# Performance work log

Hardware: AMD Instinct MI355X
Metric: run time of the kernel (lower is better)

Reference implementation:

```python
import jax, jax.numpy as jnp
import numpy as np

N_ANCHORS = 200000
TOPK = 4096          # pre-NMS top-k (standard detector practice, fixed output shape)
CONF_T = 0.5
IOU_T = 0.6


def setup_inputs() -> dict:
    key = jax.random.key(0)
    k1, k2, k3 = jax.random.split(key, 3)
    # build valid xyxy boxes: random centers in a 1024x1024 image, sizes 4..128
    cxcy = jax.random.uniform(k1, (1, N_ANCHORS, 2), minval=0.0, maxval=1024.0)
    wh = jax.random.uniform(k2, (1, N_ANCHORS, 2), minval=4.0, maxval=128.0)
    boxes = jnp.concatenate([cxcy - wh / 2, cxcy + wh / 2], axis=-1)  # [1,N,4]
    confs = jax.random.uniform(k3, (1, N_ANCHORS))                    # [1,N]
    return {"boxes": boxes, "confs": confs}


def _pairwise_iou(b):
    # b: [K,4] xyxy -> iou: [K,K]
    area = jnp.clip(b[:, 2] - b[:, 0], 0.0) * jnp.clip(b[:, 3] - b[:, 1], 0.0)
    lt = jnp.maximum(b[:, None, :2], b[None, :, :2])
    rb = jnp.minimum(b[:, None, 2:], b[None, :, 2:])
    wh = jnp.clip(rb - lt, 0.0)
    inter = wh[..., 0] * wh[..., 1]
    return inter / (area[:, None] + area[None, :] - inter + 1e-9)


def reference(boxes, confs):
    b = boxes[0]          # [N,4] single batch (module is single-batch single-class)
    c = confs[0]          # [N]
    # confidence threshold mask; invalid scores pushed below any valid score
    scores = jnp.where(c >= CONF_T, c, -1.0)
    top_scores, idx = jax.lax.top_k(scores, TOPK)   # sorted descending
    top_boxes = b[idx]                              # [K,4]
    iou = _pairwise_iou(top_boxes)                  # [K,K]
    valid_k = top_scores >= CONF_T

    # greedy sequential NMS over score-sorted candidates
    def body(i, state):
        keep, sup = state
        is_keep = jnp.logical_not(sup[i])
        keep = keep.at[i].set(is_keep)
        sup = sup | (is_keep & (iou[i] > IOU_T))
        return (keep, sup)

    keep0 = jnp.zeros((TOPK,), dtype=bool)
    keep, _ = jax.lax.fori_loop(0, TOPK, body, (keep0, jnp.logical_not(valid_k)))

    # [K,5] = x1,y1,x2,y2,conf ; suppressed rows zeroed (fixed output shape)
    out = jnp.concatenate([top_boxes, top_scores[:, None]], axis=-1)
    return jnp.where(keep[:, None], out, 0.0)
```

## Files before the change

kernel.cpp:

```cpp
#include <hip/hip_runtime.h>

#define NTOP   4096
#define SORTN  8192
#define CONF_T 0.5f
#define IOU_T  0.6f

#define HIST_OFF   0
#define CUT_OFF    8192
#define CNT_OFF    8196
#define COMP_OFF   16384
#define MEMSET_BYTES 81920
#define KEYS_OFF   131072
#define TB_OFF     2097152
#define TC_OFF     2162688
#define VALID_OFF  2179072
#define KEEP_OFF   2179584
#define MASK_OFF   4194304

typedef unsigned long long u64;
typedef unsigned int u32;

__device__ __forceinline__ void gload_lds16(const void* g, void* l) {
    __builtin_amdgcn_global_load_lds(
        (const __attribute__((address_space(1))) unsigned int*)g,
        (__attribute__((address_space(3))) unsigned int*)l, 16, 0, 0);
}

__global__ void k_keys(const float* __restrict__ confs, u64* __restrict__ keys,
                       u32* __restrict__ hist, int n) {
    int i = blockIdx.x * 256 + threadIdx.x;
    if (i >= n) return;
    float s = confs[i];
    if (s >= CONF_T) {
        u32 u = __float_as_uint(s);
        keys[i] = ((u64)u << 32) | (u32)(~i);
        int bin = (int)(u >> 12) - 0x3F000;
        bin = bin < 0 ? 0 : (bin > 2047 ? 2047 : bin);
        atomicAdd(&hist[bin], 1u);
    } else {
        keys[i] = 0ull;
    }
}

__global__ __launch_bounds__(256) void k_findcut(const u32* __restrict__ hist,
                                                 int* __restrict__ cut) {
    __shared__ u32 ch[256];
    int t = threadIdx.x;
    u32 h[8]; u32 s = 0;
#pragma unroll
    for (int k = 0; k < 8; ++k) { h[k] = hist[t * 8 + k]; s += h[k]; }
    ch[t] = s;
    __syncthreads();
    for (int off = 1; off < 256; off <<= 1) {
        u32 v = ch[t];
        u32 add = (t + off < 256) ? ch[t + off] : 0u;
        __syncthreads();
        ch[t] = v + add;
        __syncthreads();
    }
    u32 incl = ch[t];
    u32 above = incl - s;
    if (above < NTOP && incl >= NTOP) {
        u32 cum = above; int c = 0;
        for (int k = 7; k >= 0; --k) {
            cum += h[k];
            if (cum >= NTOP) { c = t * 8 + k; break; }
        }
        *cut = c;
    }
    if (t == 0 && ch[0] < NTOP) *cut = 0;
}

__global__ void k_compact(const u64* __restrict__ keys, const int* __restrict__ cut,
                          u64* __restrict__ comp, u32* __restrict__ counter, int n) {
    int i = blockIdx.x * 256 + threadIdx.x;
    if (i >= n) return;
    u64 key = keys[i];
    if (!key) return;
    int bin = (int)(u32)(key >> 44) - 0x3F000;
    bin = bin < 0 ? 0 : (bin > 2047 ? 2047 : bin);
    if (bin >= *cut) {
        u32 p = atomicAdd(counter, 1u);
        if (p < SORTN) comp[p] = key;
    }
}

__global__ __launch_bounds__(1024) void k_sort(const u64* __restrict__ comp,
                                               const float4* __restrict__ boxes,
                                               float4* __restrict__ tb,
                                               float* __restrict__ tc,
                                               u64* __restrict__ validmask) {
    __shared__ u64 sm[SORTN];
    int t = threadIdx.x;
    for (int i = t; i < SORTN; i += 1024) sm[i] = comp[i];
    __syncthreads();
    for (int k = 2; k <= SORTN; k <<= 1) {
        for (int j = k >> 1; j > 0; j >>= 1) {
            for (int i = t; i < SORTN; i += 1024) {
                int ixj = i ^ j;
                if (ixj > i) {
                    u64 a = sm[i], b = sm[ixj];
                    bool sw = ((i & k) == 0) ? (a < b) : (a > b);
                    if (sw) { sm[i] = b; sm[ixj] = a; }
                }
            }
            __syncthreads();
        }
    }
    for (int base = 0; base < NTOP; base += 1024) {
        int k = base + t;
        u64 key = sm[k];
        float score = __uint_as_float((u32)(key >> 32));
        bool valid = (key != 0ull) && (score >= CONF_T);
        float4 b = make_float4(0.f, 0.f, 0.f, 0.f);
        if (valid) {
            u32 idx = ~(u32)(key & 0xFFFFFFFFull);
            b = boxes[idx];
        }
        tb[k] = b;
        tc[k] = score;
        u64 bal = __ballot(valid);
        if ((t & 63) == 0) validmask[k >> 6] = bal;
    }
}

__global__ __launch_bounds__(256) void k_mask(const float4* __restrict__ tb,
                                              u64* __restrict__ mask) {
    __shared__ float4 cb[64];
    __shared__ float  ca[64];
    int w = blockIdx.x;
    int t = threadIdx.x;
    if (t < 64) {
        float4 b = tb[w * 64 + t];
        cb[t] = b;
        ca[t] = fmaxf(b.z - b.x, 0.f) * fmaxf(b.w - b.y, 0.f);
    }
    __syncthreads();
    int row = blockIdx.y * 256 + t;
    float4 rb = tb[row];
    float ra = fmaxf(rb.z - rb.x, 0.f) * fmaxf(rb.w - rb.y, 0.f);
    u64 m = 0;
#pragma unroll 8
    for (int j = 0; j < 64; ++j) {
        float4 c = cb[j];
        float lx = fmaxf(rb.x, c.x), ly = fmaxf(rb.y, c.y);
        float rx = fminf(rb.z, c.z), ry = fminf(rb.w, c.w);
        float iw = fmaxf(rx - lx, 0.f), ih = fmaxf(ry - ly, 0.f);
        float inter = iw * ih;
        float iou = inter / (ra + ca[j] - inter + 1e-9f);
        if (iou > IOU_T) m |= (1ull << j);
    }
    mask[(size_t)row * 64 + w] = m;
}

#define SB __builtin_amdgcn_sched_barrier(0);

#define RD(p, base) \
    p##0 = Bp[(base + 0) * 64 + lane]; p##1 = Bp[(base + 1) * 64 + lane]; \
    p##2 = Bp[(base + 2) * 64 + lane]; p##3 = Bp[(base + 3) * 64 + lane]; \
    p##4 = Bp[(base + 4) * 64 + lane]; p##5 = Bp[(base + 5) * 64 + lane]; \
    p##6 = Bp[(base + 6) * 64 + lane]; p##7 = Bp[(base + 7) * 64 + lane];

#define RL64(rv) ( ((u64)(u32)__builtin_amdgcn_readlane((int)(u32)((rv) >> 32), w) << 32) \
                 |  (u64)(u32)__builtin_amdgcn_readlane((int)(u32)(rv), w) )

#define CSTEP(rv, dv, bit) { \
    bool k_ = ((cur >> (bit)) & 1ull) == 0ull; \
    u64 mm_ = k_ ? ~0ull : 0ull;         \
    cur |= (dv) & mm_;                   \
    mysup |= (rv) & mm_;                 \
    blockkeep |= k_ ? (1ull << (bit)) : 0ull; }

#define CH(p, base) { \
    u64 d0_ = RL64(p##0), d1_ = RL64(p##1), d2_ = RL64(p##2), d3_ = RL64(p##3); \
    u64 d4_ = RL64(p##4), d5_ = RL64(p##5), d6_ = RL64(p##6), d7_ = RL64(p##7); \
    CSTEP(p##0, d0_, base + 0) CSTEP(p##1, d1_, base + 1) \
    CSTEP(p##2, d2_, base + 2) CSTEP(p##3, d3_, base + 3) \
    CSTEP(p##4, d4_, base + 4) CSTEP(p##5, d5_, base + 5) \
    CSTEP(p##6, d6_, base + 6) CSTEP(p##7, d7_, base + 7) }

__global__ __launch_bounds__(256, 1) void k_nms(const u64* __restrict__ mask,
                                                const u64* __restrict__ validmask,
                                                u64* __restrict__ keep) {
    __shared__ u64 buf[2][64 * 64];
    int tid = threadIdx.x;
    int lane = tid & 63;
    int wid = tid >> 6;

    {
        const char* src = (const char*)mask;
        char* dst = (char*)&buf[0][0];
        for (int c = wid; c < 32; c += 4)
            gload_lds16(src + c * 1024 + lane * 16, dst + c * 1024);
    }
    u64 mysup = 0, mykeep = 0;
    if (wid == 0) mysup = ~validmask[lane];
    __syncthreads();

    for (int b = 0; b < 64; ++b) {
        if (wid != 0) {
            if (b + 1 < 64) {
                const char* src = (const char*)(mask + (size_t)(b + 1) * 4096);
                char* dst = (char*)&buf[(b & 1) ^ 1][0];
                for (int c = wid - 1; c < 32; c += 3)
                    gload_lds16(src + c * 1024 + lane * 16, dst + c * 1024);
            }
        } else {
            const u64* Bp = buf[b & 1];
            int w = b;
            u32 clo = (u32)__builtin_amdgcn_readlane((int)(u32)mysup, w);
            u32 chi = (u32)__builtin_amdgcn_readlane((int)(u32)(mysup >> 32), w);
            u64 cur = ((u64)chi << 32) | clo;
            u64 blockkeep = 0;
            u64 x0, x1, x2, x3, x4, x5, x6, x7;
            u64 y0, y1, y2, y3, y4, y5, y6, y7;
            u64 z0, z1, z2, z3, z4, z5, z6, z7;
            RD(x, 0)  RD(y, 8)  SB
            RD(z, 16) SB CH(x, 0)  SB
            RD(x, 24) SB CH(y, 8)  SB
            RD(y, 32) SB CH(z, 16) SB
            RD(z, 40) SB CH(x, 24) SB
            RD(x, 48) SB CH(y, 32) SB
            RD(y, 56) SB CH(z, 40) SB
            CH(x, 48) SB
            CH(y, 56)
            if (lane == w) mykeep = blockkeep;
        }
        __syncthreads();
    }
    if (wid == 0) keep[lane] = mykeep;
}

__global__ void k_out(const float4* __restrict__ tb, const float* __restrict__ tc,
                      const u64* __restrict__ keep, float* __restrict__ out) {
    int k = blockIdx.x * 256 + threadIdx.x;
    bool kp = (keep[k >> 6] >> (k & 63)) & 1ull;
    float4 b = tb[k];
    float c = tc[k];
    float* o = out + (size_t)k * 5;
    o[0] = kp ? b.x : 0.f;
    o[1] = kp ? b.y : 0.f;
    o[2] = kp ? b.z : 0.f;
    o[3] = kp ? b.w : 0.f;
    o[4] = kp ? c : 0.f;
}

extern "C" void kernel_launch(void* const* d_in, const int* in_sizes, int n_in,
                              void* d_out, int out_size, void* d_ws, size_t ws_size,
                              hipStream_t stream) {
    const float4* boxes = (const float4*)d_in[0];
    const float*  confs = (const float*)d_in[1];
    float* out = (float*)d_out;
    char* ws = (char*)d_ws;
    int n = in_sizes[1];

    u32* hist    = (u32*)(ws + HIST_OFF);
    int* cut     = (int*)(ws + CUT_OFF);
    u32* counter = (u32*)(ws + CNT_OFF);
    u64* comp    = (u64*)(ws + COMP_OFF);
    u64* keys    = (u64*)(ws + KEYS_OFF);
    float4* tb   = (float4*)(ws + TB_OFF);
    float*  tc   = (float*)(ws + TC_OFF);
    u64* validm  = (u64*)(ws + VALID_OFF);
    u64* keep    = (u64*)(ws + KEEP_OFF);
    u64* mask    = (u64*)(ws + MASK_OFF);

    hipMemsetAsync(ws, 0, MEMSET_BYTES, stream);
    k_keys<<<(n + 255) / 256, 256, 0, stream>>>(confs, keys, hist, n);
    k_findcut<<<1, 256, 0, stream>>>(hist, cut);
    k_compact<<<(n + 255) / 256, 256, 0, stream>>>(keys, cut, comp, counter, n);
    k_sort<<<1, 1024, 0, stream>>>(comp, boxes, tb, tc, validm);
    k_mask<<<dim3(64, 16), 256, 0, stream>>>(tb, mask);
    k_nms<<<1, 256, 0, stream>>>(mask, validm, keep);
    k_out<<<16, 256, 0, stream>>>(tb, tc, keep, out);
}
```

Before: 464.4 us.

## Run NMS scan in a single wave with triple-buffered async LDS prefetch

```diff
diff --git a/kernel.cpp b/kernel.cpp
--- a/kernel.cpp
+++ b/kernel.cpp
@@ -179,56 +179,58 @@
     CSTEP(p##4, d4_, base + 4) CSTEP(p##5, d5_, base + 5) \
     CSTEP(p##6, d6_, base + 6) CSTEP(p##7, d7_, base + 7) }
 
-__global__ __launch_bounds__(256, 1) void k_nms(const u64* __restrict__ mask,
-                                                const u64* __restrict__ validmask,
-                                                u64* __restrict__ keep) {
-    __shared__ u64 buf[2][64 * 64];
-    int tid = threadIdx.x;
-    int lane = tid & 63;
-    int wid = tid >> 6;
+__global__ __launch_bounds__(64, 1) void k_nms(const u64* __restrict__ mask,
+                                               const u64* __restrict__ validmask,
+                                               u64* __restrict__ keep) {
+    __shared__ u64 buf[3][64 * 64];
+    int lane = threadIdx.x;
+    u64 mysup = ~validmask[lane];
+    u64 mykeep = 0;
 
     {
         const char* src = (const char*)mask;
-        char* dst = (char*)&buf[0][0];
-        for (int c = wid; c < 32; c += 4)
-            gload_lds16(src + c * 1024 + lane * 16, dst + c * 1024);
-    }
-    u64 mysup = 0, mykeep = 0;
-    if (wid == 0) mysup = ~validmask[lane];
-    __syncthreads();
+#pragma unroll
+        for (int c = 0; c < 32; ++c)
+            gload_lds16(src + c * 1024 + lane * 16, (char*)&buf[0][0] + c * 1024);
+#pragma unroll
+        for (int c = 0; c < 32; ++c)
+            gload_lds16(src + 32768 + c * 1024 + lane * 16, (char*)&buf[1][0] + c * 1024);
+    }
 
     for (int b = 0; b < 64; ++b) {
-        if (wid != 0) {
-            if (b + 1 < 64) {
-                const char* src = (const char*)(mask + (size_t)(b + 1) * 4096);
-                char* dst = (char*)&buf[(b & 1) ^ 1][0];
-                for (int c = wid - 1; c < 32; c += 3)
-                    gload_lds16(src + c * 1024 + lane * 16, dst + c * 1024);
-            }
-        } else {
-            const u64* Bp = buf[b & 1];
-            int w = b;
-            u32 clo = (u32)__builtin_amdgcn_readlane((int)(u32)mysup, w);
-            u32 chi = (u32)__builtin_amdgcn_readlane((int)(u32)(mysup >> 32), w);
-            u64 cur = ((u64)chi << 32) | clo;
-            u64 blockkeep = 0;
-            u64 x0, x1, x2, x3, x4, x5, x6, x7;
-            u64 y0, y1, y2, y3, y4, y5, y6, y7;
-            u64 z0, z1, z2, z3, z4, z5, z6, z7;
-            RD(x, 0)  RD(y, 8)  SB
-            RD(z, 16) SB CH(x, 0)  SB
-            RD(x, 24) SB CH(y, 8)  SB
-            RD(y, 32) SB CH(z, 16) SB
-            RD(z, 40) SB CH(x, 24) SB
-            RD(x, 48) SB CH(y, 32) SB
-            RD(y, 56) SB CH(z, 40) SB
-            CH(x, 48) SB
-            CH(y, 56)
-            if (lane == w) mykeep = blockkeep;
-        }
-        __syncthreads();
-    }
-    if (wid == 0) keep[lane] = mykeep;
+        if (b < 63) { asm volatile("s_waitcnt vmcnt(32)" ::: "memory"); }
+        else        { asm volatile("s_waitcnt vmcnt(0)"  ::: "memory"); }
+        __builtin_amdgcn_sched_barrier(0);
+
+        if (b + 2 < 64) {
+            const char* s2 = (const char*)(mask + (size_t)(b + 2) * 4096);
+            char* d2 = (char*)&buf[(b + 2) % 3][0];
+#pragma unroll
+            for (int c = 0; c < 32; ++c)
+                gload_lds16(s2 + c * 1024 + lane * 16, d2 + c * 1024);
+        }
+
+        const u64* Bp = &buf[b % 3][0];
+        int w = b;
+        u32 clo = (u32)__builtin_amdgcn_readlane((int)(u32)mysup, w);
+        u32 chi = (u32)__builtin_amdgcn_readlane((int)(u32)(mysup >> 32), w);
+        u64 cur = ((u64)chi << 32) | clo;
+        u64 blockkeep = 0;
+        u64 x0, x1, x2, x3, x4, x5, x6, x7;
+        u64 y0, y1, y2, y3, y4, y5, y6, y7;
+        u64 z0, z1, z2, z3, z4, z5, z6, z7;
+        RD(x, 0)  RD(y, 8)  SB
+        RD(z, 16) SB CH(x, 0)  SB
+        RD(x, 24) SB CH(y, 8)  SB
+        RD(y, 32) SB CH(z, 16) SB
+        RD(z, 40) SB CH(x, 24) SB
+        RD(x, 48) SB CH(y, 32) SB
+        RD(y, 56) SB CH(z, 40) SB
+        CH(x, 48) SB
+        CH(y, 56)
+        if (lane == w) mykeep = blockkeep;
+    }
+    keep[lane] = mykeep;
 }
 
 __global__ void k_out(const float4* __restrict__ tb, const float* __restrict__ tc,
@@ -271,6 +273,6 @@
     k_compact<<<(n + 255) / 256, 256, 0, stream>>>(keys, cut, comp, counter, n);
     k_sort<<<1, 1024, 0, stream>>>(comp, boxes, tb, tc, validm);
     k_mask<<<dim3(64, 16), 256, 0, stream>>>(tb, mask);
-    k_nms<<<1, 256, 0, stream>>>(mask, validm, keep);
+    k_nms<<<1, 64, 0, stream>>>(mask, validm, keep);
     k_out<<<16, 256, 0, stream>>>(tb, tc, keep, out);
 }
```

After: 478.6 us. +3.1%, slower.
